# Kernel tuning notes

Hardware: AMD Instinct MI355X
Metric: run time of the kernel (lower is better)

The kernel has to match this reference:

```python
import jax, jax.numpy as jnp
import numpy as np

B, L, D = 4, 8192, 512


def _normalize(v):
    # F.normalize: v / max(||v||, 1e-12)
    n = jnp.linalg.norm(v, axis=-1, keepdims=True)
    return v / jnp.maximum(n, 1e-12)


def setup_inputs() -> dict:
    key = jax.random.key(0)
    k1, k2, k3, k4 = jax.random.split(key, 4)
    return {
        "hidden_states": jax.random.normal(k1, (B, L, D), jnp.float32),
        "residual": jax.random.normal(k2, (B, L, D), jnp.float32),
        "q_weight": jax.random.normal(k3, (D, D), jnp.float32) * 0.02,
        "k_weight": jax.random.normal(k4, (D, D), jnp.float32) * 0.02,
        "det_state": jnp.zeros((B, D), jnp.float32),
    }


def reference(hidden_states, residual, q_weight, k_weight, det_state):
    Bs, Ls, Ds = hidden_states.shape
    # ---- CosineSimRouter.prob_boundary ----
    q = _normalize(hidden_states[:, :-1] @ q_weight.T)   # (B, L-1, D)
    k = _normalize(hidden_states[:, 1:] @ k_weight.T)    # (B, L-1, D)
    cos_sim = jnp.einsum('bld,bld->bl', q, k)            # (B, L-1)
    prob = jnp.concatenate(
        [jnp.ones((Bs, 1), jnp.float32), jnp.clip((1.0 - cos_sim) / 2.0, 0.0, 1.0)],
        axis=1)                                           # (B, L); prob[:,0]=1 (state=None path)
    token_mask = prob > 0.5                               # (B, L)

    # ---- Tokenizer: compact boundary positions (pad M -> L, static shape) ----
    counts = token_mask.sum(axis=1)                       # (B,)
    order = jnp.argsort(~token_mask, axis=1)              # stable: True-mask indices first, in order
    valid = jnp.arange(Ls)[None, :] < counts[:, None]     # (B, L)
    chunked = jnp.take_along_axis(hidden_states, order[..., None], axis=1)
    chunked = chunked * valid[..., None]                  # (B, L, D)
    chunk_probs = jnp.take_along_axis(prob, order, axis=1) * valid  # (B, L)

    # ---- DeTokenizer: EMA associative scan over compacted chunks ----
    decay = jnp.clip(1.0 - chunk_probs, 0.0, 1.0)
    # pad positions have chunk_probs=0 -> decay=1 -> state carried unchanged
    a = jnp.broadcast_to(decay[..., None], (Bs, Ls, Ds))
    b = (1.0 - decay)[..., None] * chunked
    b = b.at[:, 0].add(a[:, 0] * det_state)

    def comb(x, y):  # x earlier, y later: (a2*a1, a2*b1 + b2)
        ax, bx = x
        ay, by = y
        return ax * ay, ay * bx + by

    _, ema_out = jax.lax.associative_scan(comb, (a, b), axis=1)
    ema_out = ema_out * valid[..., None]                  # zero padded chunk slots

    # broadcast back to full sequence via cumulative chunk indexing
    chunk_idx = jnp.cumsum(token_mask.astype(jnp.int32), axis=1) - 1  # (B, L)
    ci = jnp.clip(chunk_idx, 0, Ls - 1)
    long_states = jnp.take_along_axis(ema_out, ci[..., None], axis=1)
    long_states = long_states * (chunk_idx >= 0)[..., None]

    # STE coefficient: forward == 1 (grad flows through max(1-p, p) in bwd)
    coef_raw = jnp.maximum(1.0 - prob, prob)
    coef = coef_raw + jax.lax.stop_gradient(1.0 - coef_raw)
    long_states = long_states * coef[..., None]

    output = residual + long_states                       # (B, L, D)
    return output
```

## Files before the change

### kernel.cpp

```cpp
#include <hip/hip_runtime.h>
#include <hip/hip_bf16.h>
#include <math.h>

#define B_  4
#define L_  8192
#define D_  512

#define BM   128
#define NCT  4
#define NRT  (L_ / BM)
#define KW   64
#define NSTAGE (D_ / KW)
#define BUFW 8704

#define CHUNK 64
#define NCHUNK (L_ / CHUNK)

#define MAXFIX 16380
#define FIX_TAU 1.0e-3f
#define FROWS 8
#define NSLICE 8

typedef short bf16x8 __attribute__((ext_vector_type(8)));
typedef float f32x4 __attribute__((ext_vector_type(4)));
typedef unsigned short u16;
typedef unsigned int u32;

__device__ __forceinline__ u32 pk2(float lo, float hi) {
    __hip_bfloat162 v = __float22bfloat162_rn(float2{lo, hi});
    union { __hip_bfloat162 b; u32 u; } cv; cv.b = v;
    return cv.u;
}

#define GLOAD_LDS(g, l) __builtin_amdgcn_global_load_lds( \
    (__attribute__((address_space(1))) void*)(g),         \
    (__attribute__((address_space(3))) void*)(l), 16, 0, 0)

#define NCONVB ((B_ * L_ * D_) / (256 * 8))

__global__ __launch_bounds__(256) void prep_all(
    const float* __restrict__ h, u16* __restrict__ h16,
    const float* __restrict__ wq, const float* __restrict__ wk,
    u16* __restrict__ qh, u16* __restrict__ kh,
    float* __restrict__ wqt, float* __restrict__ wkt,
    int* __restrict__ fix_cnt)
{
    __shared__ float tile[64][65];
    const int t = threadIdx.x;
    if (blockIdx.x < NCONVB) {
        size_t i = ((size_t)blockIdx.x * 256 + t) * 8;
        float4 a = *(const float4*)(h + i);
        float4 b = *(const float4*)(h + i + 4);
        uint4 v;
        v.x = pk2(a.x, a.y); v.y = pk2(a.z, a.w);
        v.z = pk2(b.x, b.y); v.w = pk2(b.z, b.w);
        *(uint4*)(h16 + i) = v;
        return;
    }
    const int wb = blockIdx.x - NCONVB;
    const int bi = wb & 7;
    const int bj = wb >> 3;
    if (wb == 0 && t == 0) *fix_cnt = 0;
    const int c0 = bi * 64, k0 = bj * 64;
    const float* src = wq; float* dst = wqt; u16* dsth = qh;
#pragma unroll
    for (int m = 0; m < 2; ++m) {
        __syncthreads();
#pragma unroll
        for (int it = 0; it < 4; ++it) {
            int r = it * 16 + (t >> 4);
            int cc = (t & 15) * 4;
            float4 v = *(const float4*)(src + (size_t)(c0 + r) * D_ + k0 + cc);
            tile[r][cc] = v.x; tile[r][cc + 1] = v.y;
            tile[r][cc + 2] = v.z; tile[r][cc + 3] = v.w;
            uint2 hv; hv.x = pk2(v.x, v.y); hv.y = pk2(v.z, v.w);
            *(uint2*)(dsth + (size_t)(c0 + r) * D_ + k0 + cc) = hv;
        }
        __syncthreads();
#pragma unroll
        for (int it = 0; it < 4; ++it) {
            int cl = t & 63;
            int kq = it * 4 + (t >> 6);
            float4 v;
            v.x = tile[cl][kq * 4 + 0]; v.y = tile[cl][kq * 4 + 1];
            v.z = tile[cl][kq * 4 + 2]; v.w = tile[cl][kq * 4 + 3];
            size_t o = ((size_t)((k0 >> 2) + kq) * 512 + (c0 + cl)) * 4;
            *(float4*)(dst + o) = v;
        }
        src = wk; dst = wkt; dsth = kh;
    }
}

__global__ __launch_bounds__(256, 2) void qk_mfma(
    const u16* __restrict__ h16,
    const u16* __restrict__ wqh, const u16* __restrict__ wkh,
    float* __restrict__ part)
{
    const int bid = blockIdx.x;
    const int swz = (bid & 7) * 128 + (bid >> 3);
    const int ct = swz & 3, rt = (swz >> 2) & 63, b = swz >> 8;
    const int t = threadIdx.x, wid = t >> 6, lane = t & 63;
    const int l15 = lane & 15, l4 = lane >> 4;

    __shared__ __align__(16) u16 ah[3 * BUFW];
    __shared__ float red[4][BM][3];

    const int r0 = rt * BM;
    const u16* hb = h16 + (size_t)b * L_ * D_;

    const int rl0 = wid * 32 + (lane >> 3);
    const int csw = ((lane & 7) ^ ((lane >> 3) & 7)) * 8;
    const u16* gA = hb + (size_t)(r0 + rl0) * D_ + csw;
    const int dstw = wid * 32 * 64;
    const u16* gE = hb + (size_t)(r0 + 128 + (lane >> 3)) * D_ + (lane & 7) * 8;

    const int colb = ct * 128 + wid * 32;
    const u16* bq0 = wqh + (size_t)(colb + l15) * D_ + l4 * 8;
    const u16* bq1 = bq0 + (size_t)16 * D_;
    const u16* bk0 = wkh + (size_t)(colb + l15) * D_ + l4 * 8;
    const u16* bk1 = bk0 + (size_t)16 * D_;

    int aoff[8];
#pragma unroll
    for (int rf = 0; rf < 8; ++rf) {
        int R = rf * 16 + l15;
        aoff[rf] = R * 64 + ((l4 ^ (R & 7)) * 8);
    }
    const int aoffE = 128 * 64 + l4 * 8;

    f32x4 accq[8][2], acck[8][2], ackl[2];
    const f32x4 zero = {0.f, 0.f, 0.f, 0.f};
#pragma unroll
    for (int rf = 0; rf < 8; ++rf) {
        accq[rf][0] = zero; accq[rf][1] = zero;
        acck[rf][0] = zero; acck[rf][1] = zero;
    }
    ackl[0] = zero; ackl[1] = zero;

#define STAGE_ISSUE(S, BUF) do { const size_t _o = (size_t)(S) * KW;  \
    u16* _d = &ah[(BUF) * BUFW];                                      \
    GLOAD_LDS(gA + _o,         _d + dstw);                            \
    GLOAD_LDS(gA + _o + 4096,  _d + dstw + 512);                      \
    GLOAD_LDS(gA + _o + 8192,  _d + dstw + 1024);                     \
    GLOAD_LDS(gA + _o + 12288, _d + dstw + 1536);                     \
    if (wid == 0) GLOAD_LDS(gE + _o, _d + 8192); } while (0)

    STAGE_ISSUE(0, 0);
    STAGE_ISSUE(1, 1);

    for (int s = 0; s < NSTAGE; ++s) {
        if (s < NSTAGE - 1) {
            asm volatile("s_waitcnt vmcnt(4)" ::: "memory");
        } else {
            asm volatile("s_waitcnt vmcnt(0)" ::: "memory");
        }
        __builtin_amdgcn_sched_barrier(0);
        __builtin_amdgcn_s_barrier();
        __builtin_amdgcn_sched_barrier(0);

        const int so = s * KW;
        bf16x8 q00 = *(const bf16x8*)(bq0 + so);
        bf16x8 q01 = *(const bf16x8*)(bq0 + so + 32);
        bf16x8 q10 = *(const bf16x8*)(bq1 + so);
        bf16x8 q11 = *(const bf16x8*)(bq1 + so + 32);
        bf16x8 k00 = *(const bf16x8*)(bk0 + so);
        bf16x8 k01 = *(const bf16x8*)(bk0 + so + 32);
        bf16x8 k10 = *(const bf16x8*)(bk1 + so);
        bf16x8 k11 = *(const bf16x8*)(bk1 + so + 32);
        __builtin_amdgcn_sched_barrier(0);

        if (s + 2 < NSTAGE) STAGE_ISSUE(s + 2, (s + 2) % 3);
        __builtin_amdgcn_sched_barrier(0);

        const u16* ab = &ah[(s % 3) * BUFW];
#pragma unroll
        for (int kk = 0; kk < 2; ++kk) {
            bf16x8 fq0 = kk ? q01 : q00;
            bf16x8 fq1 = kk ? q11 : q10;
            bf16x8 fk0 = kk ? k01 : k00;
            bf16x8 fk1 = kk ? k11 : k10;
#pragma unroll
            for (int rf = 0; rf < 8; ++rf) {
                bf16x8 a = *(const bf16x8*)(ab + (aoff[rf] ^ (kk * 32)));
                accq[rf][0] = __builtin_amdgcn_mfma_f32_16x16x32_bf16(a, fq0, accq[rf][0], 0, 0, 0);
                accq[rf][1] = __builtin_amdgcn_mfma_f32_16x16x32_bf16(a, fq1, accq[rf][1], 0, 0, 0);
                acck[rf][0] = __builtin_amdgcn_mfma_f32_16x16x32_bf16(a, fk0, acck[rf][0], 0, 0, 0);
                acck[rf][1] = __builtin_amdgcn_mfma_f32_16x16x32_bf16(a, fk1, acck[rf][1], 0, 0, 0);
            }
            bf16x8 al = *(const bf16x8*)(ab + (aoffE ^ (kk * 32)));
            ackl[0] = __builtin_amdgcn_mfma_f32_16x16x32_bf16(al, fk0, ackl[0], 0, 0, 0);
            ackl[1] = __builtin_amdgcn_mfma_f32_16x16x32_bf16(al, fk1, ackl[1], 0, 0, 0);
        }
    }
#undef STAGE_ISSUE

#pragma unroll
    for (int rf = 0; rf < 8; ++rf) {
#pragma unroll
        for (int reg = 0; reg < 4; ++reg) {
            float pq = 0.f, pk = 0.f, pd = 0.f;
#pragma unroll
            for (int cf = 0; cf < 2; ++cf) {
                float qv = accq[rf][cf][reg];
                float kv = acck[rf][cf][reg];
                pq += qv * qv;
                pk += kv * kv;
                float ksh;
                if (reg < 3) {
                    ksh = acck[rf][cf][reg + 1];
                } else {
                    float up = __shfl(acck[rf][cf][0], (lane + 16) & 63);
                    float nx0 = (rf < 7) ? acck[rf + 1][cf][0] : ackl[cf][0];
                    float nx = __shfl(nx0, l15);
                    ksh = (l4 == 3) ? nx : up;
                }
                pd += qv * ksh;
            }
#pragma unroll
            for (int off = 1; off < 16; off <<= 1) {
                pq += __shfl_xor(pq, off);
                pk += __shfl_xor(pk, off);
                pd += __shfl_xor(pd, off);
            }
            if (l15 == 0) {
                int row = rf * 16 + l4 * 4 + reg;
                red[wid][row][0] = pq;
                red[wid][row][1] = pk;
                red[wid][row][2] = pd;
            }
        }
    }
    __syncthreads();
    if (t < BM) {
        float pq = red[0][t][0] + red[1][t][0] + red[2][t][0] + red[3][t][0];
        float pk = red[0][t][1] + red[1][t][1] + red[2][t][1] + red[3][t][1];
        float pd = red[0][t][2] + red[1][t][2] + red[2][t][2] + red[3][t][2];
        size_t o = (((size_t)ct * B_ + b) * L_ + (r0 + t)) * 3;
        part[o + 0] = pq; part[o + 1] = pk; part[o + 2] = pd;
    }
}

__global__ __launch_bounds__(256) void cos_reduce(
    const float* __restrict__ part, float* __restrict__ p,
    int* __restrict__ fix_cnt, int* __restrict__ fix_list)
{
    int idx = blockIdx.x * 256 + threadIdx.x;
    if (idx >= B_ * L_) return;
    int b = idx / L_;
    int tp = idx % L_;
    if (tp == 0) { p[idx] = 1.0f; return; }
    int l = tp - 1;
    float nq = 0.f, nk = 0.f, dt = 0.f;
#pragma unroll
    for (int ct = 0; ct < NCT; ++ct) {
        size_t o = (((size_t)ct * B_ + b) * L_ + l) * 3;
        nq += part[o + 0];
        dt += part[o + 2];
        nk += part[o + 4];
    }
    float qn = sqrtf(nq); if (qn < 1e-12f) qn = 1e-12f;
    float kn = sqrtf(nk); if (kn < 1e-12f) kn = 1e-12f;
    float cs = dt / (qn * kn);
    float pr = 0.5f * (1.0f - cs);
    pr = fminf(fmaxf(pr, 0.0f), 1.0f);
    p[idx] = pr;
    if (fabsf(cs) < FIX_TAU) {
        int slot = atomicAdd(fix_cnt, 1);
        if (slot < MAXFIX) fix_list[slot] = idx;
    }
}

__global__ __launch_bounds__(256) void fixup_main(
    const float* __restrict__ h,
    const float* __restrict__ wqt, const float* __restrict__ wkt,
    const int* __restrict__ fix_cnt, const int* __restrict__ fix_list,
    float* __restrict__ part_fix)
{
    __shared__ float hq[FROWS][D_];
    __shared__ float hk[FROWS][D_];
    __shared__ float red[FROWS][3][4];
    const int t = threadIdx.x, wid = t >> 6, lane = t & 63;
    const int col16 = lane & 15, kpart = lane >> 4;
    int n = *fix_cnt; if (n > MAXFIX) n = MAXFIX;
    const int ntiles = (n + FROWS - 1) / FROWS;
    const int nitems = ntiles * NSLICE;

    for (int item = blockIdx.x; item < nitems; item += gridDim.x) {
        const int tile = item >> 3;
        const int cs = item & 7;
        __syncthreads();
#pragma unroll
        for (int r = 0; r < FROWS; ++r) {
            int s = tile * FROWS + r;
            int idx = fix_list[s < n ? s : 0];
            int bb = idx >> 13;
            int tp = idx & (L_ - 1);
            const float* hr = h + ((size_t)bb * L_ + (tp - 1)) * D_;
            ((float2*)hq[r])[t] = ((const float2*)hr)[t];
            ((float2*)hk[r])[t] = ((const float2*)(hr + D_))[t];
        }
        __syncthreads();

        const int c = cs * 64 + wid * 16 + col16;
        float qa0, qa1, qa2, qa3, qa4, qa5, qa6, qa7;
        float ka0, ka1, ka2, ka3, ka4, ka5, ka6, ka7;
        qa0=qa1=qa2=qa3=qa4=qa5=qa6=qa7=0.f;
        ka0=ka1=ka2=ka3=ka4=ka5=ka6=ka7=0.f;

        const int k0 = kpart * 32;
        float4 wv = *(const float4*)(wqt + ((size_t)k0 * 512 + c) * 4);
        float4 xv = *(const float4*)(wkt + ((size_t)k0 * 512 + c) * 4);
#pragma unroll 4
        for (int kq = k0; kq < k0 + 32; ++kq) {
            const int kn = (kq + 1 < k0 + 32) ? kq + 1 : kq;
            float4 wn = *(const float4*)(wqt + ((size_t)kn * 512 + c) * 4);
            float4 xn = *(const float4*)(wkt + ((size_t)kn * 512 + c) * 4);
#define FROW(R, QA, KA) { \
            float4 hv = *(const float4*)(&hq[R][kq * 4]); \
            float4 kv = *(const float4*)(&hk[R][kq * 4]); \
            QA += hv.x*wv.x + hv.y*wv.y + hv.z*wv.z + hv.w*wv.w; \
            KA += kv.x*xv.x + kv.y*xv.y + kv.z*xv.z + kv.w*xv.w; }
            FROW(0, qa0, ka0) FROW(1, qa1, ka1) FROW(2, qa2, ka2) FROW(3, qa3, ka3)
            FROW(4, qa4, ka4) FROW(5, qa5, ka5) FROW(6, qa6, ka6) FROW(7, qa7, ka7)
#undef FROW
            wv = wn; xv = xn;
        }

#define REDROW(R, QA, KA) { \
        float qf = QA; qf += __shfl_xor(qf, 16); qf += __shfl_xor(qf, 32); \
        float kf = KA; kf += __shfl_xor(kf, 16); kf += __shfl_xor(kf, 32); \
        float pq = qf * qf, pk = kf * kf, pd = qf * kf; \
        pq += __shfl_xor(pq, 1); pk += __shfl_xor(pk, 1); pd += __shfl_xor(pd, 1); \
        pq += __shfl_xor(pq, 2); pk += __shfl_xor(pk, 2); pd += __shfl_xor(pd, 2); \
        pq += __shfl_xor(pq, 4); pk += __shfl_xor(pk, 4); pd += __shfl_xor(pd, 4); \
        pq += __shfl_xor(pq, 8); pk += __shfl_xor(pk, 8); pd += __shfl_xor(pd, 8); \
        if (lane == 0) { red[R][0][wid] = pq; red[R][1][wid] = pk; red[R][2][wid] = pd; } }
        REDROW(0, qa0, ka0) REDROW(1, qa1, ka1) REDROW(2, qa2, ka2) REDROW(3, qa3, ka3)
        REDROW(4, qa4, ka4) REDROW(5, qa5, ka5) REDROW(6, qa6, ka6) REDROW(7, qa7, ka7)
#undef REDROW
        __syncthreads();
        if (t < FROWS) {
            int s = tile * FROWS + t;
            if (s < n) {
                float* pp = part_fix + ((size_t)s * NSLICE + cs) * 3;
                pp[0] = red[t][0][0] + red[t][0][1] + red[t][0][2] + red[t][0][3];
                pp[1] = red[t][1][0] + red[t][1][1] + red[t][1][2] + red[t][1][3];
                pp[2] = red[t][2][0] + red[t][2][1] + red[t][2][2] + red[t][2][3];
            }
        }
    }
}

__global__ __launch_bounds__(256) void fixup_final(
    const int* __restrict__ fix_cnt, const int* __restrict__ fix_list,
    const float* __restrict__ part_fix, float* __restrict__ p)
{
    int n = *fix_cnt; if (n > MAXFIX) n = MAXFIX;
    for (int s = blockIdx.x * 256 + threadIdx.x; s < n; s += gridDim.x * 256) {
        float nq = 0.f, nk = 0.f, dt = 0.f;
#pragma unroll
        for (int cs = 0; cs < NSLICE; ++cs) {
            const float* pp = part_fix + ((size_t)s * NSLICE + cs) * 3;
            nq += pp[0]; nk += pp[1]; dt += pp[2];
        }
        float qn = sqrtf(nq); if (qn < 1e-12f) qn = 1e-12f;
        float kn = sqrtf(nk); if (kn < 1e-12f) kn = 1e-12f;
        float cs2 = dt / (qn * kn);
        float pr = 0.5f * (1.0f - cs2);
        pr = fminf(fmaxf(pr, 0.0f), 1.0f);
        p[fix_list[s]] = pr;
    }
}

__global__ __launch_bounds__(256) void scan_a(
    const float* __restrict__ h, const float* __restrict__ p,
    float* __restrict__ Bc, float* __restrict__ Ac)
{
    const int t = threadIdx.x;
    const int c = blockIdx.x, b = blockIdx.y;
    const int l0 = c * CHUNK;
    const float* pb = p + (size_t)b * L_ + l0;
    const float2* hb = (const float2*)(h + ((size_t)b * L_ + l0) * D_) + t;

    float2 st = {0.f, 0.f};
    float ap = 1.f;
#pragma unroll 4
    for (int i = 0; i < CHUNK; ++i) {
        float pr = pb[i];
        float2 hv = hb[(size_t)i * 256];
        bool sel = pr > 0.5f;
        float a = sel ? 1.f - pr : 1.f;
        float g = sel ? pr : 0.f;
        st.x = a * st.x + g * hv.x;
        st.y = a * st.y + g * hv.y;
        ap *= a;
    }
    ((float2*)Bc)[((size_t)b * NCHUNK + c) * 256 + t] = st;
    if (t == 0) Ac[b * NCHUNK + c] = ap;
}

__global__ __launch_bounds__(256) void scan_b(
    const float* __restrict__ Ac, const float* __restrict__ Bc,
    const float* __restrict__ det, float* __restrict__ carry)
{
    const int t = threadIdx.x;
    const int b = blockIdx.x;
    const float* acb = Ac + b * NCHUNK;
    const float2* bcb = (const float2*)Bc + (size_t)b * NCHUNK * 256 + t;
    float2* cb = (float2*)carry + (size_t)b * NCHUNK * 256 + t;
    float2 st = ((const float2*)det)[(size_t)b * 256 + t];

    float a0 = acb[0], a1 = acb[1], a2 = acb[2], a3 = acb[3];
    float2 b0 = bcb[0], b1 = bcb[256], b2 = bcb[512], b3 = bcb[768];
    for (int g = 0; g < NCHUNK / 4; ++g) {
        const int nc = (g + 1 < NCHUNK / 4) ? (g + 1) * 4 : g * 4;
        float an0 = acb[nc], an1 = acb[nc + 1], an2 = acb[nc + 2], an3 = acb[nc + 3];
        float2 bn0 = bcb[(size_t)nc * 256],        bn1 = bcb[(size_t)(nc + 1) * 256];
        float2 bn2 = bcb[(size_t)(nc + 2) * 256],  bn3 = bcb[(size_t)(nc + 3) * 256];
        const size_t c0 = (size_t)g * 4 * 256;
        cb[c0]       = st; st.x = a0 * st.x + b0.x; st.y = a0 * st.y + b0.y;
        cb[c0 + 256] = st; st.x = a1 * st.x + b1.x; st.y = a1 * st.y + b1.y;
        cb[c0 + 512] = st; st.x = a2 * st.x + b2.x; st.y = a2 * st.y + b2.y;
        cb[c0 + 768] = st; st.x = a3 * st.x + b3.x; st.y = a3 * st.y + b3.y;
        a0 = an0; a1 = an1; a2 = an2; a3 = an3;
        b0 = bn0; b1 = bn1; b2 = bn2; b3 = bn3;
    }
}

__global__ __launch_bounds__(256) void scan_c(
    const float* __restrict__ h, const float* __restrict__ p,
    const float* __restrict__ res, const float* __restrict__ carry,
    float* __restrict__ out)
{
    const int t = threadIdx.x;
    const int c = blockIdx.x, b = blockIdx.y;
    const int l0 = c * CHUNK;
    const float* pb = p + (size_t)b * L_ + l0;
    const size_t base = ((size_t)b * L_ + l0) * 256 + t;
    const float2* hb = (const float2*)h + base;
    const float2* rb = (const float2*)res + base;
    float2* ob = (float2*)out + base;

    float2 st = ((const float2*)carry)[((size_t)b * NCHUNK + c) * 256 + t];
#pragma unroll 4
    for (int i = 0; i < CHUNK; ++i) {
        float pr = pb[i];
        float2 hv = hb[(size_t)i * 256];
        float2 rv = rb[(size_t)i * 256];
        bool sel = pr > 0.5f;
        float a = sel ? 1.f - pr : 1.f;
        float g = sel ? pr : 0.f;
        st.x = a * st.x + g * hv.x;
        st.y = a * st.y + g * hv.y;
        float2 ov; ov.x = rv.x + st.x; ov.y = rv.y + st.y;
        ob[(size_t)i * 256] = ov;
    }
}

extern "C" void kernel_launch(void* const* d_in, const int* in_sizes, int n_in,
                              void* d_out, int out_size, void* d_ws, size_t ws_size,
                              hipStream_t stream)
{
    const float* h   = (const float*)d_in[0];
    const float* res = (const float*)d_in[1];
    const float* wq  = (const float*)d_in[2];
    const float* wk  = (const float*)d_in[3];
    const float* det = (const float*)d_in[4];
    float* out = (float*)d_out;

    u16* h16 = (u16*)d_out;

    float* ws = (float*)d_ws;
    float* part  = ws;
    float* p     = part + (size_t)NCT * B_ * L_ * 3;
    float* Ac    = p + (size_t)B_ * L_;
    float* Bc    = Ac + (size_t)B_ * NCHUNK;
    float* carry = Bc + (size_t)B_ * NCHUNK * D_;
    int*  fix_cnt  = (int*)(carry + (size_t)B_ * NCHUNK * D_);
    int*  fix_list = fix_cnt + 4;
    u16* wqh = (u16*)(fix_list + MAXFIX);
    u16* wkh = wqh + (size_t)D_ * D_;
    float* wqt = (float*)(wkh + (size_t)D_ * D_);
    float* wkt = wqt + (size_t)D_ * D_;
    float* part_fix = wkt + (size_t)D_ * D_;

    prep_all<<<NCONVB + 64, 256, 0, stream>>>(h, h16, wq, wk, wqh, wkh,
                                              wqt, wkt, fix_cnt);
    qk_mfma<<<NCT * NRT * B_, 256, 0, stream>>>(h16, wqh, wkh, part);
    cos_reduce<<<(B_ * L_ + 255) / 256, 256, 0, stream>>>(part, p, fix_cnt, fix_list);
    fixup_main<<<1024, 256, 0, stream>>>(h, wqt, wkt, fix_cnt, fix_list, part_fix);
    fixup_final<<<64, 256, 0, stream>>>(fix_cnt, fix_list, part_fix, p);
    scan_a<<<dim3(NCHUNK, B_), 256, 0, stream>>>(h, p, Bc, Ac);
    scan_b<<<B_, 256, 0, stream>>>(Ac, Bc, det, carry);
    scan_c<<<dim3(NCHUNK, B_), 256, 0, stream>>>(h, p, res, carry, out);
}
```

Baseline: 169.3 us.

## Split QK projection into 8 column tiles and alias LDS reduction buffer

The QK MFMA kernel now splits the 512 output columns into 8 tiles of 64 instead of 4 tiles of 128, so each wave holds one 16-column fragment. This halves the accumulator registers and doubles the grid, aiming for better occupancy and more blocks across CUs. The reduction scratch now shares LDS with the staging buffers through a union, with an extra barrier so the two uses do not overlap. The cost is that every hidden-state tile is loaded twice as many times, and the reducer has twice as many partials to sum.

New measurement: 181.2 us. 7.1% more time.

```diff
diff --git a/kernel.cpp b/kernel.cpp
--- a/kernel.cpp
+++ b/kernel.cpp
@@ -7,7 +7,7 @@
 #define D_  512
 
 #define BM   128
-#define NCT  4
+#define NCT  8
 #define NRT  (L_ / BM)
 #define KW   64
 #define NSTAGE (D_ / KW)
@@ -97,13 +97,15 @@
     float* __restrict__ part)
 {
     const int bid = blockIdx.x;
-    const int swz = (bid & 7) * 128 + (bid >> 3);
-    const int ct = swz & 3, rt = (swz >> 2) & 63, b = swz >> 8;
+    const int swz = (bid & 7) * 256 + (bid >> 3);
+    const int ct = swz & 7, rt = (swz >> 3) & 63, b = swz >> 9;
     const int t = threadIdx.x, wid = t >> 6, lane = t & 63;
     const int l15 = lane & 15, l4 = lane >> 4;
 
-    __shared__ __align__(16) u16 ah[3 * BUFW];
-    __shared__ float red[4][BM][3];
+    __shared__ __align__(16) union ShMem {
+        u16 ah[3 * BUFW];
+        float red[4][BM][3];
+    } sh;
 
     const int r0 = rt * BM;
     const u16* hb = h16 + (size_t)b * L_ * D_;
@@ -114,11 +116,9 @@
     const int dstw = wid * 32 * 64;
     const u16* gE = hb + (size_t)(r0 + 128 + (lane >> 3)) * D_ + (lane & 7) * 8;
 
-    const int colb = ct * 128 + wid * 32;
+    const int colb = ct * 64 + wid * 16;
     const u16* bq0 = wqh + (size_t)(colb + l15) * D_ + l4 * 8;
-    const u16* bq1 = bq0 + (size_t)16 * D_;
     const u16* bk0 = wkh + (size_t)(colb + l15) * D_ + l4 * 8;
-    const u16* bk1 = bk0 + (size_t)16 * D_;
 
     int aoff[8];
 #pragma unroll
@@ -128,17 +128,14 @@
     }
     const int aoffE = 128 * 64 + l4 * 8;
 
-    f32x4 accq[8][2], acck[8][2], ackl[2];
+    f32x4 accq[8], acck[8], ackl;
     const f32x4 zero = {0.f, 0.f, 0.f, 0.f};
 #pragma unroll
-    for (int rf = 0; rf < 8; ++rf) {
-        accq[rf][0] = zero; accq[rf][1] = zero;
-        acck[rf][0] = zero; acck[rf][1] = zero;
-    }
-    ackl[0] = zero; ackl[1] = zero;
+    for (int rf = 0; rf < 8; ++rf) { accq[rf] = zero; acck[rf] = zero; }
+    ackl = zero;
 
 #define STAGE_ISSUE(S, BUF) do { const size_t _o = (size_t)(S) * KW;  \
-    u16* _d = &ah[(BUF) * BUFW];                                      \
+    u16* _d = &sh.ah[(BUF) * BUFW];                                   \
     GLOAD_LDS(gA + _o,         _d + dstw);                            \
     GLOAD_LDS(gA + _o + 4096,  _d + dstw + 512);                      \
     GLOAD_LDS(gA + _o + 8192,  _d + dstw + 1024);                     \
@@ -161,61 +158,50 @@
         const int so = s * KW;
         bf16x8 q00 = *(const bf16x8*)(bq0 + so);
         bf16x8 q01 = *(const bf16x8*)(bq0 + so + 32);
-        bf16x8 q10 = *(const bf16x8*)(bq1 + so);
-        bf16x8 q11 = *(const bf16x8*)(bq1 + so + 32);
         bf16x8 k00 = *(const bf16x8*)(bk0 + so);
         bf16x8 k01 = *(const bf16x8*)(bk0 + so + 32);
-        bf16x8 k10 = *(const bf16x8*)(bk1 + so);
-        bf16x8 k11 = *(const bf16x8*)(bk1 + so + 32);
         __builtin_amdgcn_sched_barrier(0);
 
         if (s + 2 < NSTAGE) STAGE_ISSUE(s + 2, (s + 2) % 3);
         __builtin_amdgcn_sched_barrier(0);
 
-        const u16* ab = &ah[(s % 3) * BUFW];
+        const u16* ab = &sh.ah[(s % 3) * BUFW];
 #pragma unroll
         for (int kk = 0; kk < 2; ++kk) {
-            bf16x8 fq0 = kk ? q01 : q00;
-            bf16x8 fq1 = kk ? q11 : q10;
-            bf16x8 fk0 = kk ? k01 : k00;
-            bf16x8 fk1 = kk ? k11 : k10;
+            bf16x8 fq = kk ? q01 : q00;
+            bf16x8 fk = kk ? k01 : k00;
 #pragma unroll
             for (int rf = 0; rf < 8; ++rf) {
                 bf16x8 a = *(const bf16x8*)(ab + (aoff[rf] ^ (kk * 32)));
-                accq[rf][0] = __builtin_amdgcn_mfma_f32_16x16x32_bf16(a, fq0, accq[rf][0], 0, 0, 0);
-                accq[rf][1] = __builtin_amdgcn_mfma_f32_16x16x32_bf16(a, fq1, accq[rf][1], 0, 0, 0);
-                acck[rf][0] = __builtin_amdgcn_mfma_f32_16x16x32_bf16(a, fk0, acck[rf][0], 0, 0, 0);
-                acck[rf][1] = __builtin_amdgcn_mfma_f32_16x16x32_bf16(a, fk1, acck[rf][1], 0, 0, 0);
+                accq[rf] = __builtin_amdgcn_mfma_f32_16x16x32_bf16(a, fq, accq[rf], 0, 0, 0);
+                acck[rf] = __builtin_amdgcn_mfma_f32_16x16x32_bf16(a, fk, acck[rf], 0, 0, 0);
             }
             bf16x8 al = *(const bf16x8*)(ab + (aoffE ^ (kk * 32)));
-            ackl[0] = __builtin_amdgcn_mfma_f32_16x16x32_bf16(al, fk0, ackl[0], 0, 0, 0);
-            ackl[1] = __builtin_amdgcn_mfma_f32_16x16x32_bf16(al, fk1, ackl[1], 0, 0, 0);
+            ackl = __builtin_amdgcn_mfma_f32_16x16x32_bf16(al, fk, ackl, 0, 0, 0);
         }
     }
 #undef STAGE_ISSUE
 
+    __syncthreads();
+
 #pragma unroll
     for (int rf = 0; rf < 8; ++rf) {
 #pragma unroll
         for (int reg = 0; reg < 4; ++reg) {
-            float pq = 0.f, pk = 0.f, pd = 0.f;
-#pragma unroll
-            for (int cf = 0; cf < 2; ++cf) {
-                float qv = accq[rf][cf][reg];
-                float kv = acck[rf][cf][reg];
-                pq += qv * qv;
-                pk += kv * kv;
-                float ksh;
-                if (reg < 3) {
-                    ksh = acck[rf][cf][reg + 1];
-                } else {
-                    float up = __shfl(acck[rf][cf][0], (lane + 16) & 63);
-                    float nx0 = (rf < 7) ? acck[rf + 1][cf][0] : ackl[cf][0];
-                    float nx = __shfl(nx0, l15);
-                    ksh = (l4 == 3) ? nx : up;
-                }
-                pd += qv * ksh;
+            float qv = accq[rf][reg];
+            float kv = acck[rf][reg];
+            float pq = qv * qv;
+            float pk = kv * kv;
+            float ksh;
+            if (reg < 3) {
+                ksh = acck[rf][reg + 1];
+            } else {
+                float up = __shfl(acck[rf][0], (lane + 16) & 63);
+                float nx0 = (rf < 7) ? acck[rf + 1][0] : ackl[0];
+                float nx = __shfl(nx0, l15);
+                ksh = (l4 == 3) ? nx : up;
             }
+            float pd = qv * ksh;
 #pragma unroll
             for (int off = 1; off < 16; off <<= 1) {
                 pq += __shfl_xor(pq, off);
@@ -224,17 +210,17 @@
             }
             if (l15 == 0) {
                 int row = rf * 16 + l4 * 4 + reg;
-                red[wid][row][0] = pq;
-                red[wid][row][1] = pk;
-                red[wid][row][2] = pd;
+                sh.red[wid][row][0] = pq;
+                sh.red[wid][row][1] = pk;
+                sh.red[wid][row][2] = pd;
             }
         }
     }
     __syncthreads();
     if (t < BM) {
-        float pq = red[0][t][0] + red[1][t][0] + red[2][t][0] + red[3][t][0];
-        float pk = red[0][t][1] + red[1][t][1] + red[2][t][1] + red[3][t][1];
-        float pd = red[0][t][2] + red[1][t][2] + red[2][t][2] + red[3][t][2];
+        float pq = sh.red[0][t][0] + sh.red[1][t][0] + sh.red[2][t][0] + sh.red[3][t][0];
+        float pk = sh.red[0][t][1] + sh.red[1][t][1] + sh.red[2][t][1] + sh.red[3][t][1];
+        float pd = sh.red[0][t][2] + sh.red[1][t][2] + sh.red[2][t][2] + sh.red[3][t][2];
         size_t o = (((size_t)ct * B_ + b) * L_ + (r0 + t)) * 3;
         part[o + 0] = pq; part[o + 1] = pk; part[o + 2] = pd;
     }
```
